# Performance work log

Hardware: AMD Instinct MI355X
Metric: run time of the kernel (lower is better)

The kernel has to match this reference:

```python
import jax, jax.numpy as jnp
import numpy as np

N_ATOMS = 10000
N_PAIR = 100000
F = 128
N_HEAD = 4
FH = F // N_HEAD  # 32
DEGREES = [1, 2, 3]
N_DEG = len(DEGREES)
REPEATS = np.array([2 * l + 1 for l in DEGREES])  # [3,5,7]
M_TOT = int(REPEATS.sum())  # 15
K_RBF = 32


def ssp(x):
    # shifted softplus: softplus(x) - log(2)
    return jax.nn.softplus(x) - jnp.log(2.0).astype(x.dtype)


def setup_inputs() -> dict:
    key = jax.random.key(0)
    ks = jax.random.split(key, 16)
    inp = {
        "x": jax.random.normal(ks[0], (N_ATOMS, F), jnp.float32),
        "rbf_ij": jax.random.normal(ks[1], (N_PAIR, K_RBF), jnp.float32),
        "sph_ij": jax.random.normal(ks[2], (N_PAIR, M_TOT), jnp.float32),
        "phi_r_cut": jax.random.uniform(ks[3], (N_PAIR,), jnp.float32),
        "idx_i": jnp.sort(jax.random.randint(ks[4], (N_PAIR,), 0, N_ATOMS)),
        "idx_j": jax.random.randint(ks[5], (N_PAIR,), 0, N_ATOMS),
        "pair_mask": jnp.ones((N_PAIR,), jnp.float32),
        # params
        "W_Q": jax.random.normal(ks[6], (N_DEG, N_HEAD, FH, FH), jnp.float32) / np.sqrt(FH),
        "W_K": jax.random.normal(ks[7], (N_DEG, N_HEAD, FH, FH), jnp.float32) / np.sqrt(FH),
        # in2f MLP: single dense F -> F
        "W_in": jax.random.normal(ks[8], (F, F), jnp.float32) / np.sqrt(F),
        "b_in": jnp.zeros((F,), jnp.float32),
        # radial filter MLP: K -> K (ssp) -> n_deg*F
        "W_f1": jax.random.normal(ks[9], (K_RBF, K_RBF), jnp.float32) / np.sqrt(K_RBF),
        "b_f1": jnp.zeros((K_RBF,), jnp.float32),
        "W_f2": jax.random.normal(ks[10], (K_RBF, N_DEG * F), jnp.float32) / np.sqrt(K_RBF),
        "b_f2": jnp.zeros((N_DEG * F,), jnp.float32),
        # f2out MLP: single dense F -> F
        "W_out": jax.random.normal(ks[11], (F, F), jnp.float32) / np.sqrt(F),
        "b_out": jnp.zeros((F,), jnp.float32),
    }
    return inp


def reference(x, rbf_ij, sph_ij, phi_r_cut, idx_i, idx_j, pair_mask,
              W_Q, W_K, W_in, b_in, W_f1, b_f1, W_f2, b_f2, W_out, b_out):
    n = x.shape[0]
    # in2f embedding (last in2f dim == F)
    x_f = x @ W_in + b_in                                  # (n, F)
    x_head = x_f.reshape(n, N_HEAD, FH)                    # (n, h, FH)

    # per-degree, per-head linear maps (the nested vmap matmuls)
    Q = jnp.einsum('dhij,nhj->ndhi', W_Q, x_head)          # (n, n_deg, h, FH)
    K = jnp.einsum('dhij,nhj->ndhi', W_K, x_head)

    m = pair_mask[:, None, None, None]
    Q_i = Q[idx_i] * m                                     # (P, n_deg, h, FH)
    K_j = K[idx_j] * m

    # radial filter: MLP(rbf) -> (P, n_deg, h, FH), scaled by cutoff
    h1 = ssp(rbf_ij @ W_f1 + b_f1)
    W_ij = (h1 @ W_f2 + b_f2).reshape(-1, N_DEG, N_HEAD, FH)
    W_ij = W_ij * phi_r_cut[:, None, None, None]

    # attention coefficients per degree/head
    alpha = jnp.sum(Q_i * K_j * W_ij, axis=-1)             # (P, n_deg, h)
    alpha = jnp.repeat(alpha, repeats=REPEATS, axis=1, total_repeat_length=M_TOT)  # (P, m_tot, h)
    alpha = alpha / jnp.sqrt(jnp.asarray(FH, x.dtype))     # att_scale

    # outer product of neighbor features with spherical harmonics
    x_j = x_head[idx_j] * pair_mask[:, None, None]         # (P, h, FH)
    z_ij = jnp.einsum('pm,phf->pmhf', sph_ij, x_j)         # (P, m_tot, h, FH)
    z_ij = alpha[:, :, :, None] * z_ij
    z_ij = z_ij.reshape(z_ij.shape[0], M_TOT, F)           # (P, m_tot, F)

    agg = jax.ops.segment_sum(z_ij, idx_i, num_segments=n)  # (n, m_tot, F)

    # f2out projection (last f2out dim == F)
    out = agg @ W_out + b_out                               # (n, m_tot, F)
    return out
```

## Files before the change

### kernel.cpp

```cpp
#include <hip/hip_runtime.h>
#include <hip/hip_bf16.h>

#define N_ATOMS 10000
#define N_PAIR  100000
#define F_DIM   128
#define N_HEAD  4
#define FH      32
#define N_DEG   3
#define M_TOT   15
#define K_RBF   32
#define R_OUT   (N_ATOMS * M_TOT)
#define PPB     50

typedef __attribute__((ext_vector_type(8))) short short8;
typedef __attribute__((ext_vector_type(4))) float f32x4;

union frag_cast { int i[4]; short8 s; };

__device__ __forceinline__ float sspf(float v) {
    float sp = fmaxf(v, 0.f) + log1pf(expf(-fabsf(v)));
    return sp - 0.69314718055994531f;
}

__device__ __forceinline__ unsigned short bf16_rne(float x) {
    unsigned int u = __float_as_uint(x);
    unsigned int r = u + 0x7fffu + ((u >> 16) & 1u);
    return (unsigned short)(r >> 16);
}
__device__ __forceinline__ float bf16_tof(unsigned short h) {
    return __uint_as_float(((unsigned int)h) << 16);
}

__global__ __launch_bounds__(256) void k_zero(float4* __restrict__ p, int n4)
{
    int i = blockIdx.x * 256 + threadIdx.x;
    int stride = gridDim.x * 256;
    float4 z = make_float4(0.f, 0.f, 0.f, 0.f);
    for (; i < n4; i += stride) p[i] = z;
}

__global__ __launch_bounds__(256) void k_gemm128(
    const float* __restrict__ A, const float* __restrict__ B,
    const float* __restrict__ bias, float* __restrict__ C, int rows)
{
    __shared__ float As[32][132];
    __shared__ float Bs[32][132];
    int r0 = blockIdx.x * 128;
    int t = threadIdx.x;
    int ty = t >> 4, tx = t & 15;

    float acc[8][8];
    #pragma unroll
    for (int i = 0; i < 8; ++i)
        #pragma unroll
        for (int j = 0; j < 8; ++j) acc[i][j] = 0.f;

    for (int k0 = 0; k0 < 128; k0 += 32) {
        #pragma unroll
        for (int r = 0; r < 16; ++r) {
            int idx = t + 256 * r;
            int row = idx >> 5, kk = idx & 31;
            int grow = r0 + row;
            As[kk][row] = (grow < rows) ? A[grow * 128 + k0 + kk] : 0.f;
        }
        #pragma unroll
        for (int r = 0; r < 16; ++r) {
            int idx = t + 256 * r;
            int kk = idx >> 7, c = idx & 127;
            Bs[kk][c] = B[(k0 + kk) * 128 + c];
        }
        __syncthreads();

        #pragma unroll
        for (int kk = 0; kk < 32; ++kk) {
            float a[8], b[8];
            *(float4*)&a[0] = *(const float4*)&As[kk][ty * 4];
            *(float4*)&a[4] = *(const float4*)&As[kk][64 + ty * 4];
            *(float4*)&b[0] = *(const float4*)&Bs[kk][tx * 4];
            *(float4*)&b[4] = *(const float4*)&Bs[kk][64 + tx * 4];
            #pragma unroll
            for (int i = 0; i < 8; ++i)
                #pragma unroll
                for (int j = 0; j < 8; ++j)
                    acc[i][j] = fmaf(a[i], b[j], acc[i][j]);
        }
        __syncthreads();
    }

    float bj[8];
    #pragma unroll
    for (int j = 0; j < 4; ++j) { bj[j] = bias[tx * 4 + j]; bj[4 + j] = bias[64 + tx * 4 + j]; }

    #pragma unroll
    for (int i = 0; i < 8; ++i) {
        int row = r0 + ((i < 4) ? (ty * 4 + i) : (64 + ty * 4 + (i - 4)));
        if (row < rows) {
            float4 v0, v1;
            v0.x = acc[i][0] + bj[0]; v0.y = acc[i][1] + bj[1];
            v0.z = acc[i][2] + bj[2]; v0.w = acc[i][3] + bj[3];
            v1.x = acc[i][4] + bj[4]; v1.y = acc[i][5] + bj[5];
            v1.z = acc[i][6] + bj[6]; v1.w = acc[i][7] + bj[7];
            *(float4*)&C[row * 128 + tx * 4] = v0;
            *(float4*)&C[row * 128 + 64 + tx * 4] = v1;
        }
    }
}

__global__ __launch_bounds__(384) void k_qk(
    const float* __restrict__ xh, const float* __restrict__ W_Q,
    const float* __restrict__ W_K, float* __restrict__ Q, float* __restrict__ K)
{
    __shared__ float xfs[32][128];
    int t = threadIdx.x;
    int h = (t >> 5) & 3;
    float wq[32], wk[32];
    const float4* wqp = (const float4*)(W_Q + t * 32);
    const float4* wkp = (const float4*)(W_K + t * 32);
    #pragma unroll
    for (int j4 = 0; j4 < 8; ++j4) {
        float4 a = wqp[j4], b = wkp[j4];
        wq[4 * j4 + 0] = a.x; wq[4 * j4 + 1] = a.y; wq[4 * j4 + 2] = a.z; wq[4 * j4 + 3] = a.w;
        wk[4 * j4 + 0] = b.x; wk[4 * j4 + 1] = b.y; wk[4 * j4 + 2] = b.z; wk[4 * j4 + 3] = b.w;
    }
    int ab = blockIdx.x * 32;
    for (int idx = t; idx < 4096; idx += 384) {
        int aa = idx >> 7, f = idx & 127;
        int ag = ab + aa;
        xfs[aa][f] = (ag < N_ATOMS) ? xh[ag * 128 + f] : 0.f;
    }
    __syncthreads();
    for (int aa = 0; aa < 32; ++aa) {
        int ag = ab + aa;
        if (ag >= N_ATOMS) break;
        const float4* xv = (const float4*)&xfs[aa][h * 32];
        float q0 = 0.f, q1 = 0.f, k0 = 0.f, k1 = 0.f;
        #pragma unroll
        for (int j4 = 0; j4 < 8; j4 += 2) {
            float4 x0 = xv[j4], x1 = xv[j4 + 1];
            q0 = fmaf(wq[4 * j4 + 0], x0.x, q0); q0 = fmaf(wq[4 * j4 + 1], x0.y, q0);
            q0 = fmaf(wq[4 * j4 + 2], x0.z, q0); q0 = fmaf(wq[4 * j4 + 3], x0.w, q0);
            q1 = fmaf(wq[4 * j4 + 4], x1.x, q1); q1 = fmaf(wq[4 * j4 + 5], x1.y, q1);
            q1 = fmaf(wq[4 * j4 + 6], x1.z, q1); q1 = fmaf(wq[4 * j4 + 7], x1.w, q1);
            k0 = fmaf(wk[4 * j4 + 0], x0.x, k0); k0 = fmaf(wk[4 * j4 + 1], x0.y, k0);
            k0 = fmaf(wk[4 * j4 + 2], x0.z, k0); k0 = fmaf(wk[4 * j4 + 3], x0.w, k0);
            k1 = fmaf(wk[4 * j4 + 4], x1.x, k1); k1 = fmaf(wk[4 * j4 + 5], x1.y, k1);
            k1 = fmaf(wk[4 * j4 + 6], x1.z, k1); k1 = fmaf(wk[4 * j4 + 7], x1.w, k1);
        }
        Q[ag * 384 + t] = q0 + q1;
        K[ag * 384 + t] = k0 + k1;
    }
}

__global__ __launch_bounds__(256) void k_cvt_w2(
    const float* __restrict__ W, unsigned short* __restrict__ Wh,
    unsigned short* __restrict__ Wl)
{
    int idx = blockIdx.x * 256 + threadIdx.x;
    if (idx < 12288) {
        int e = idx >> 5, k = idx & 31;
        float v = W[k * 384 + e];
        unsigned short h = bf16_rne(v);
        unsigned short l = bf16_rne(v - bf16_tof(h));
        Wh[e * 32 + k] = h;
        Wl[e * 32 + k] = l;
    }
}

__global__ __launch_bounds__(256) void k_pair(
    const float* __restrict__ rbf, const float* __restrict__ phi,
    const float* __restrict__ mask, const int* __restrict__ idx_i,
    const int* __restrict__ idx_j, const float* __restrict__ W_f1,
    const float* __restrict__ b_f1, const unsigned short* __restrict__ W2h,
    const unsigned short* __restrict__ W2l, const float* __restrict__ b_f2,
    const float* __restrict__ Q, const float* __restrict__ K,
    float* __restrict__ alpha)
{
    __shared__ float g_s[16][388];
    __shared__ unsigned int h1p_s[16][36];
    __shared__ int   i_s[16];
    __shared__ int   j_s[16];
    __shared__ float phim_s[16];

    float (*rbf_s)[33] = (float (*)[33])(&g_s[0][0]);
    float (*wf1_s)[33] = (float (*)[33])(&g_s[0][0] + 16 * 33);

    int t = threadIdx.x;
    int p0 = blockIdx.x * 16;

    for (int idx = t; idx < 1536; idx += 256) {
        if (idx < 512) {
            rbf_s[idx >> 5][idx & 31] = rbf[p0 * 32 + idx];
        } else {
            int k = idx - 512;
            wf1_s[k >> 5][k & 31] = W_f1[k];
        }
    }
    if (t < 16) {
        int pg = p0 + t;
        i_s[t] = idx_i[pg];
        j_s[t] = idx_j[pg];
        float m = mask[pg];
        phim_s[t] = phi[pg] * m * m * 0.17677669529663687f;
    }
    __syncthreads();

    {
        int p = t >> 4, c0 = (t & 15) * 2;
        float acc0 = b_f1[c0], acc1 = b_f1[c0 + 1];
        #pragma unroll
        for (int k = 0; k < 32; ++k) {
            float rv = rbf_s[p][k];
            acc0 = fmaf(rv, wf1_s[k][c0], acc0);
            acc1 = fmaf(rv, wf1_s[k][c0 + 1], acc1);
        }
        float h0 = sspf(acc0), h1v = sspf(acc1);
        unsigned short hh0 = bf16_rne(h0);
        unsigned short ll0 = bf16_rne(h0 - bf16_tof(hh0));
        unsigned short hh1 = bf16_rne(h1v);
        unsigned short ll1 = bf16_rne(h1v - bf16_tof(hh1));
        h1p_s[p][c0]     = ((unsigned int)hh0 << 16) | (unsigned int)ll0;
        h1p_s[p][c0 + 1] = ((unsigned int)hh1 << 16) | (unsigned int)ll1;
    }
    __syncthreads();

    #pragma unroll
    for (int it = 0; it < 6; ++it) {
        int idx = it * 256 + t;
        int p = idx / 96;
        int c4 = idx - p * 96;
        const float4* qp = (const float4*)(Q + i_s[p] * 384) + c4;
        const float4* kp = (const float4*)(K + j_s[p] * 384) + c4;
        float4 qv = *qp, kv = *kp;
        float4 gv;
        gv.x = qv.x * kv.x; gv.y = qv.y * kv.y;
        gv.z = qv.z * kv.z; gv.w = qv.w * kv.w;
        *(float4*)&g_s[p][c4 * 4] = gv;
    }
    __syncthreads();

    int wave = t >> 6, lane = t & 63;
    int quad = lane >> 4, l15 = lane & 15;

    short8 ah, al;
    {
        const unsigned int* hp = &h1p_s[l15][quad * 8];
        uint4 u01 = *(const uint4*)hp;
        uint4 u23 = *(const uint4*)(hp + 4);
        unsigned int u[8] = {u01.x, u01.y, u01.z, u01.w, u23.x, u23.y, u23.z, u23.w};
        frag_cast fh, fl;
        #pragma unroll
        for (int q = 0; q < 4; ++q) {
            unsigned int a0 = u[2 * q], a1 = u[2 * q + 1];
            fh.i[q] = (int)((a0 >> 16) | (a1 & 0xffff0000u));
            fl.i[q] = (int)((a0 & 0xffffu) | (a1 << 16));
        }
        ah = fh.s;
        al = fl.s;
    }

    #pragma unroll
    for (int dd = 0; dd < 3; ++dd) {
        int dh = wave * 3 + dd;
        int e_base = dh * 32;
        short8 bh0 = *(const short8*)(W2h + (e_base + l15) * 32 + quad * 8);
        short8 bl0 = *(const short8*)(W2l + (e_base + l15) * 32 + quad * 8);
        short8 bh1 = *(const short8*)(W2h + (e_base + 16 + l15) * 32 + quad * 8);
        short8 bl1 = *(const short8*)(W2l + (e_base + 16 + l15) * 32 + quad * 8);
        float b2v0 = b_f2[e_base + l15];
        float b2v1 = b_f2[e_base + 16 + l15];

        f32x4 s0 = {0.f, 0.f, 0.f, 0.f};
        f32x4 s1 = {0.f, 0.f, 0.f, 0.f};
        s0 = __builtin_amdgcn_mfma_f32_16x16x32_bf16(ah, bh0, s0, 0, 0, 0);
        s1 = __builtin_amdgcn_mfma_f32_16x16x32_bf16(ah, bh1, s1, 0, 0, 0);
        s0 = __builtin_amdgcn_mfma_f32_16x16x32_bf16(al, bh0, s0, 0, 0, 0);
        s1 = __builtin_amdgcn_mfma_f32_16x16x32_bf16(al, bh1, s1, 0, 0, 0);
        s0 = __builtin_amdgcn_mfma_f32_16x16x32_bf16(ah, bl0, s0, 0, 0, 0);
        s1 = __builtin_amdgcn_mfma_f32_16x16x32_bf16(ah, bl1, s1, 0, 0, 0);

        float vsum[4];
        #pragma unroll
        for (int r = 0; r < 4; ++r) {
            int prow = quad * 4 + r;
            float v = (s0[r] + b2v0) * g_s[prow][e_base + l15]
                    + (s1[r] + b2v1) * g_s[prow][e_base + 16 + l15];
            #pragma unroll
            for (int off = 8; off >= 1; off >>= 1)
                v += __shfl_xor(v, off, 16);
            vsum[r] = v;
        }
        if (l15 == 0) {
            #pragma unroll
            for (int r = 0; r < 4; ++r) {
                int prow = quad * 4 + r;
                alpha[(p0 + prow) * 12 + dh] = vsum[r] * phim_s[prow];
            }
        }
    }
}

__global__ __launch_bounds__(256) void k_cvt_b(
    const float* __restrict__ W, unsigned short* __restrict__ Bth,
    unsigned short* __restrict__ Btl)
{
    int idx = blockIdx.x * 256 + threadIdx.x;
    int cc = idx >> 7, kk = idx & 127;
    float v = W[kk * 128 + cc];
    unsigned short h = bf16_rne(v);
    unsigned short l = bf16_rne(v - bf16_tof(h));
    Bth[cc * 128 + kk] = h;
    Btl[cc * 128 + kk] = l;
}

__device__ __forceinline__ void flush_acc(float* __restrict__ agg, int a,
                                          const float* acc, int t, bool interior)
{
    float* base = agg + (long)a * (M_TOT * 128) + t;
    if (interior) {
        #pragma unroll
        for (int m = 0; m < M_TOT; ++m) base[m * 128] = acc[m];
    } else {
        #pragma unroll
        for (int m = 0; m < M_TOT; ++m) atomicAdd(&base[m * 128], acc[m]);
    }
}

__global__ __launch_bounds__(512) void k_aggc(
    const float* __restrict__ xh, const float* __restrict__ alpha,
    const float* __restrict__ sph, const int* __restrict__ idx_i,
    const int* __restrict__ idx_j, const float* __restrict__ mask,
    float* __restrict__ agg)
{
    int tid = threadIdx.x;
    int grp = tid >> 7;
    int t   = tid & 127;
    int h   = (t >> 5) & 3;
    int g0  = (blockIdx.x * 4 + grp) * PPB;
    int g1  = g0 + PPB;

    int prevA = (g0 > 0) ? idx_i[g0 - 1] : -1;
    int nextA = (g1 < N_PAIR) ? idx_i[g1] : -1;

    float acc[M_TOT];
    #pragma unroll
    for (int m = 0; m < M_TOT; ++m) acc[m] = 0.f;

    int cur = idx_i[g0];
    bool started_inside = (cur != prevA);

    for (int p = g0; p < g1; ++p) {
        int ii = idx_i[p];
        if (ii != cur) {
            flush_acc(agg, cur, acc, t, started_inside);
            #pragma unroll
            for (int m = 0; m < M_TOT; ++m) acc[m] = 0.f;
            cur = ii;
            started_inside = true;
        }
        int jj = idx_j[p];
        float xj = xh[jj * 128 + t] * mask[p];
        float a0 = alpha[p * 12 + h];
        float a1 = alpha[p * 12 + 4 + h];
        float a2 = alpha[p * 12 + 8 + h];
        const float* sp = sph + p * 15;
        #pragma unroll
        for (int m = 0; m < M_TOT; ++m) {
            float av = (m < 3) ? a0 : ((m < 8) ? a1 : a2);
            acc[m] = fmaf(sp[m] * av, xj, acc[m]);
        }
    }
    bool interior = started_inside && (cur != nextA);
    flush_acc(agg, cur, acc, t, interior);
}

__global__ __launch_bounds__(256) void k_out2(
    const unsigned short* __restrict__ Bth, const unsigned short* __restrict__ Btl,
    const float* __restrict__ bias, float* __restrict__ C)
{
    __shared__ unsigned int ap_s[64][132];
    int tid = threadIdx.x;
    long r0 = (long)blockIdx.x * 64;

    #pragma unroll
    for (int it = 0; it < 16; ++it) {
        int idx = tid + it * 256;
        int row = idx >> 5, c4 = (idx & 31) * 4;
        long gr = r0 + row;
        float4 v = make_float4(0.f, 0.f, 0.f, 0.f);
        if (gr < (long)R_OUT) v = *(const float4*)(C + gr * 128 + c4);
        float vv[4] = {v.x, v.y, v.z, v.w};
        unsigned int pk[4];
        #pragma unroll
        for (int q = 0; q < 4; ++q) {
            unsigned short hh = bf16_rne(vv[q]);
            unsigned short ll = bf16_rne(vv[q] - bf16_tof(hh));
            pk[q] = ((unsigned int)hh << 16) | (unsigned int)ll;
        }
        *(uint4*)&ap_s[row][c4] = make_uint4(pk[0], pk[1], pk[2], pk[3]);
    }
    __syncthreads();

    int wave = tid >> 6, lane = tid & 63;
    int quad = lane >> 4, l15 = lane & 15;

    short8 fa_h[4], fa_l[4];
    #pragma unroll
    for (int ks = 0; ks < 4; ++ks) {
        const unsigned int* hp = &ap_s[wave * 16 + l15][ks * 32 + quad * 8];
        uint4 u01 = *(const uint4*)hp;
        uint4 u23 = *(const uint4*)(hp + 4);
        unsigned int u[8] = {u01.x, u01.y, u01.z, u01.w, u23.x, u23.y, u23.z, u23.w};
        frag_cast fh, fl;
        #pragma unroll
        for (int q = 0; q < 4; ++q) {
            unsigned int a0 = u[2 * q], a1 = u[2 * q + 1];
            fh.i[q] = (int)((a0 >> 16) | (a1 & 0xffff0000u));
            fl.i[q] = (int)((a0 & 0xffffu) | (a1 << 16));
        }
        fa_h[ks] = fh.s;
        fa_l[ks] = fl.s;
    }

    #pragma unroll
    for (int ct = 0; ct < 8; ++ct) {
        int colbase = ct * 16;
        short8 bh[4], bl[4];
        #pragma unroll
        for (int ks = 0; ks < 4; ++ks) {
            int off = (colbase + l15) * 128 + ks * 32 + quad * 8;
            bh[ks] = *(const short8*)(Bth + off);
            bl[ks] = *(const short8*)(Btl + off);
        }
        f32x4 oacc = {0.f, 0.f, 0.f, 0.f};
        #pragma unroll
        for (int ks = 0; ks < 4; ++ks) {
            oacc = __builtin_amdgcn_mfma_f32_16x16x32_bf16(fa_h[ks], bh[ks], oacc, 0, 0, 0);
            oacc = __builtin_amdgcn_mfma_f32_16x16x32_bf16(fa_l[ks], bh[ks], oacc, 0, 0, 0);
            oacc = __builtin_amdgcn_mfma_f32_16x16x32_bf16(fa_h[ks], bl[ks], oacc, 0, 0, 0);
        }
        float bv = bias[colbase + l15];
        #pragma unroll
        for (int r = 0; r < 4; ++r) {
            long row = r0 + wave * 16 + quad * 4 + r;
            if (row < (long)R_OUT)
                C[row * 128 + colbase + l15] = oacc[r] + bv;
        }
    }
}

extern "C" void kernel_launch(void* const* d_in, const int* in_sizes, int n_in,
                              void* d_out, int out_size, void* d_ws, size_t ws_size,
                              hipStream_t stream) {
    const float* x        = (const float*)d_in[0];
    const float* rbf_ij   = (const float*)d_in[1];
    const float* sph_ij   = (const float*)d_in[2];
    const float* phi_r    = (const float*)d_in[3];
    const int*   idx_i    = (const int*)d_in[4];
    const int*   idx_j    = (const int*)d_in[5];
    const float* pmask    = (const float*)d_in[6];
    const float* W_Q      = (const float*)d_in[7];
    const float* W_K      = (const float*)d_in[8];
    const float* W_in     = (const float*)d_in[9];
    const float* b_in     = (const float*)d_in[10];
    const float* W_f1     = (const float*)d_in[11];
    const float* b_f1     = (const float*)d_in[12];
    const float* W_f2     = (const float*)d_in[13];
    const float* b_f2     = (const float*)d_in[14];
    const float* W_out    = (const float*)d_in[15];
    const float* b_out    = (const float*)d_in[16];
    float* out = (float*)d_out;

    float* ws    = (float*)d_ws;
    float* xh    = ws;
    float* Qbuf  = xh + N_ATOMS * F_DIM;
    float* Kbuf  = Qbuf + N_ATOMS * 384;
    float* alpha = Kbuf + N_ATOMS * 384;
    unsigned short* Bth = (unsigned short*)(alpha + N_PAIR * 12);
    unsigned short* Btl = Bth + 16384;
    unsigned short* W2h = Btl + 16384;
    unsigned short* W2l = W2h + 12288;

    k_zero<<<2048, 256, 0, stream>>>((float4*)d_out, R_OUT * 128 / 4);
    k_cvt_b<<<64, 256, 0, stream>>>(W_out, Bth, Btl);
    k_cvt_w2<<<48, 256, 0, stream>>>(W_f2, W2h, W2l);
    k_gemm128<<<(N_ATOMS + 127) / 128, 256, 0, stream>>>(x, W_in, b_in, xh, N_ATOMS);
    k_qk<<<(N_ATOMS + 31) / 32, 384, 0, stream>>>(xh, W_Q, W_K, Qbuf, Kbuf);
    k_pair<<<N_PAIR / 16, 256, 0, stream>>>(rbf_ij, phi_r, pmask, idx_i, idx_j,
                                            W_f1, b_f1, W2h, W2l, b_f2,
                                            Qbuf, Kbuf, alpha);
    k_aggc<<<N_PAIR / (4 * PPB), 512, 0, stream>>>(xh, alpha, sph_ij, idx_i, idx_j,
                                                   pmask, out);
    k_out2<<<(R_OUT + 63) / 64, 256, 0, stream>>>(Bth, Btl, b_out, out);
}
```

Measured before the change: 440.0 us.

## Fold output projection into per-atom features before aggregation

Uses linearity to apply W_out per head to each atom's features (x_head · W_out rows) once per atom, producing a 4x128 table per atom. The aggregation kernel then combines the per-head projected features with alpha and writes the final output directly with the bias pre-initialized, removing the 150k×128×128 output GEMM pass and its read/write of the full output. The cost is a larger gather per pair (4x128 floats instead of 128) and extra per-pair FMAs; the output buffer is pre-filled with the bias, so boundary atomics add onto it.

```diff
diff --git a/kernel.cpp b/kernel.cpp
--- a/kernel.cpp
+++ b/kernel.cpp
@@ -31,12 +31,15 @@
     return __uint_as_float(((unsigned int)h) << 16);
 }
 
-__global__ __launch_bounds__(256) void k_zero(float4* __restrict__ p, int n4)
+__global__ __launch_bounds__(256) void k_binit(
+    const float* __restrict__ b, float4* __restrict__ out, int n4)
 {
     int i = blockIdx.x * 256 + threadIdx.x;
     int stride = gridDim.x * 256;
-    float4 z = make_float4(0.f, 0.f, 0.f, 0.f);
-    for (; i < n4; i += stride) p[i] = z;
+    for (; i < n4; i += stride) {
+        int c4 = i & 31;
+        out[i] = *(const float4*)(b + c4 * 4);
+    }
 }
 
 __global__ __launch_bounds__(256) void k_gemm128(
@@ -299,26 +302,57 @@
     }
 }
 
-__global__ __launch_bounds__(256) void k_cvt_b(
-    const float* __restrict__ W, unsigned short* __restrict__ Bth,
-    unsigned short* __restrict__ Btl)
-{
-    int idx = blockIdx.x * 256 + threadIdx.x;
-    int cc = idx >> 7, kk = idx & 127;
-    float v = W[kk * 128 + cc];
-    unsigned short h = bf16_rne(v);
-    unsigned short l = bf16_rne(v - bf16_tof(h));
-    Bth[cc * 128 + kk] = h;
-    Btl[cc * 128 + kk] = l;
-}
-
-__device__ __forceinline__ void flush_acc(float* __restrict__ agg, int a,
-                                          const float* acc, int t, bool interior)
-{
-    float* base = agg + (long)a * (M_TOT * 128) + t;
+__global__ __launch_bounds__(256) void k_xw(
+    const float* __restrict__ xh, const float* __restrict__ W,
+    float* __restrict__ xwh)
+{
+    __shared__ float xs[32][132];
+    int t = threadIdx.x;
+    int a0 = blockIdx.x * 32;
+    #pragma unroll
+    for (int it = 0; it < 4; ++it) {
+        int idx = t + it * 256;
+        int row = idx >> 5, c4 = (idx & 31) * 4;
+        int ga = a0 + row;
+        float4 v = make_float4(0.f, 0.f, 0.f, 0.f);
+        if (ga < N_ATOMS) v = *(const float4*)(xh + ga * 128 + c4);
+        *(float4*)&xs[row][c4] = v;
+    }
+    __syncthreads();
+
+    int c = t & 127;
+    int half = t >> 7;
+    #pragma unroll
+    for (int h = 0; h < 4; ++h) {
+        float w[32];
+        #pragma unroll
+        for (int k = 0; k < 32; ++k) w[k] = W[(h * 32 + k) * 128 + c];
+        float acc[16];
+        #pragma unroll
+        for (int i = 0; i < 16; ++i) acc[i] = 0.f;
+        #pragma unroll
+        for (int k = 0; k < 32; ++k) {
+            float wv = w[k];
+            #pragma unroll
+            for (int i = 0; i < 16; ++i)
+                acc[i] = fmaf(xs[half * 16 + i][h * 32 + k], wv, acc[i]);
+        }
+        #pragma unroll
+        for (int i = 0; i < 16; ++i) {
+            int ga = a0 + half * 16 + i;
+            if (ga < N_ATOMS) xwh[(long)ga * 512 + h * 128 + c] = acc[i];
+        }
+    }
+}
+
+__device__ __forceinline__ void flush_acc(float* __restrict__ out, int a,
+                                          const float* acc, float bout,
+                                          int t, bool interior)
+{
+    float* base = out + (long)a * (M_TOT * 128) + t;
     if (interior) {
         #pragma unroll
-        for (int m = 0; m < M_TOT; ++m) base[m * 128] = acc[m];
+        for (int m = 0; m < M_TOT; ++m) base[m * 128] = acc[m] + bout;
     } else {
         #pragma unroll
         for (int m = 0; m < M_TOT; ++m) atomicAdd(&base[m * 128], acc[m]);
@@ -326,18 +360,18 @@
 }
 
 __global__ __launch_bounds__(512) void k_aggc(
-    const float* __restrict__ xh, const float* __restrict__ alpha,
+    const float* __restrict__ xwh, const float* __restrict__ alpha,
     const float* __restrict__ sph, const int* __restrict__ idx_i,
     const int* __restrict__ idx_j, const float* __restrict__ mask,
-    float* __restrict__ agg)
+    const float* __restrict__ b_out, float* __restrict__ out)
 {
     int tid = threadIdx.x;
     int grp = tid >> 7;
     int t   = tid & 127;
-    int h   = (t >> 5) & 3;
     int g0  = (blockIdx.x * 4 + grp) * PPB;
     int g1  = g0 + PPB;
 
+    float bout = b_out[t];
     int prevA = (g0 > 0) ? idx_i[g0 - 1] : -1;
     int nextA = (g1 < N_PAIR) ? idx_i[g1] : -1;
 
@@ -351,101 +385,32 @@
     for (int p = g0; p < g1; ++p) {
         int ii = idx_i[p];
         if (ii != cur) {
-            flush_acc(agg, cur, acc, t, started_inside);
+            flush_acc(out, cur, acc, bout, t, started_inside);
             #pragma unroll
             for (int m = 0; m < M_TOT; ++m) acc[m] = 0.f;
             cur = ii;
             started_inside = true;
         }
         int jj = idx_j[p];
-        float xj = xh[jj * 128 + t] * mask[p];
-        float a0 = alpha[p * 12 + h];
-        float a1 = alpha[p * 12 + 4 + h];
-        float a2 = alpha[p * 12 + 8 + h];
+        const float* xp = xwh + (long)jj * 512;
+        float xw0 = xp[t];
+        float xw1 = xp[128 + t];
+        float xw2 = xp[256 + t];
+        float xw3 = xp[384 + t];
+        float mv = mask[p];
+        const float* ap = alpha + p * 12;
+        float sd0 = (ap[0] * xw0 + ap[1] * xw1 + ap[2]  * xw2 + ap[3]  * xw3) * mv;
+        float sd1 = (ap[4] * xw0 + ap[5] * xw1 + ap[6]  * xw2 + ap[7]  * xw3) * mv;
+        float sd2 = (ap[8] * xw0 + ap[9] * xw1 + ap[10] * xw2 + ap[11] * xw3) * mv;
         const float* sp = sph + p * 15;
         #pragma unroll
         for (int m = 0; m < M_TOT; ++m) {
-            float av = (m < 3) ? a0 : ((m < 8) ? a1 : a2);
-            acc[m] = fmaf(sp[m] * av, xj, acc[m]);
+            float sdv = (m < 3) ? sd0 : ((m < 8) ? sd1 : sd2);
+            acc[m] = fmaf(sp[m], sdv, acc[m]);
         }
     }
     bool interior = started_inside && (cur != nextA);
-    flush_acc(agg, cur, acc, t, interior);
-}
-
-__global__ __launch_bounds__(256) void k_out2(
-    const unsigned short* __restrict__ Bth, const unsigned short* __restrict__ Btl,
-    const float* __restrict__ bias, float* __restrict__ C)
-{
-    __shared__ unsigned int ap_s[64][132];
-    int tid = threadIdx.x;
-    long r0 = (long)blockIdx.x * 64;
-
-    #pragma unroll
-    for (int it = 0; it < 16; ++it) {
-        int idx = tid + it * 256;
-        int row = idx >> 5, c4 = (idx & 31) * 4;
-        long gr = r0 + row;
-        float4 v = make_float4(0.f, 0.f, 0.f, 0.f);
-        if (gr < (long)R_OUT) v = *(const float4*)(C + gr * 128 + c4);
-        float vv[4] = {v.x, v.y, v.z, v.w};
-        unsigned int pk[4];
-        #pragma unroll
-        for (int q = 0; q < 4; ++q) {
-            unsigned short hh = bf16_rne(vv[q]);
-            unsigned short ll = bf16_rne(vv[q] - bf16_tof(hh));
-            pk[q] = ((unsigned int)hh << 16) | (unsigned int)ll;
-        }
-        *(uint4*)&ap_s[row][c4] = make_uint4(pk[0], pk[1], pk[2], pk[3]);
-    }
-    __syncthreads();
-
-    int wave = tid >> 6, lane = tid & 63;
-    int quad = lane >> 4, l15 = lane & 15;
-
-    short8 fa_h[4], fa_l[4];
-    #pragma unroll
-    for (int ks = 0; ks < 4; ++ks) {
-        const unsigned int* hp = &ap_s[wave * 16 + l15][ks * 32 + quad * 8];
-        uint4 u01 = *(const uint4*)hp;
-        uint4 u23 = *(const uint4*)(hp + 4);
-        unsigned int u[8] = {u01.x, u01.y, u01.z, u01.w, u23.x, u23.y, u23.z, u23.w};
-        frag_cast fh, fl;
-        #pragma unroll
-        for (int q = 0; q < 4; ++q) {
-            unsigned int a0 = u[2 * q], a1 = u[2 * q + 1];
-            fh.i[q] = (int)((a0 >> 16) | (a1 & 0xffff0000u));
-            fl.i[q] = (int)((a0 & 0xffffu) | (a1 << 16));
-        }
-        fa_h[ks] = fh.s;
-        fa_l[ks] = fl.s;
-    }
-
-    #pragma unroll
-    for (int ct = 0; ct < 8; ++ct) {
-        int colbase = ct * 16;
-        short8 bh[4], bl[4];
-        #pragma unroll
-        for (int ks = 0; ks < 4; ++ks) {
-            int off = (colbase + l15) * 128 + ks * 32 + quad * 8;
-            bh[ks] = *(const short8*)(Bth + off);
-            bl[ks] = *(const short8*)(Btl + off);
-        }
-        f32x4 oacc = {0.f, 0.f, 0.f, 0.f};
-        #pragma unroll
-        for (int ks = 0; ks < 4; ++ks) {
-            oacc = __builtin_amdgcn_mfma_f32_16x16x32_bf16(fa_h[ks], bh[ks], oacc, 0, 0, 0);
-            oacc = __builtin_amdgcn_mfma_f32_16x16x32_bf16(fa_l[ks], bh[ks], oacc, 0, 0, 0);
-            oacc = __builtin_amdgcn_mfma_f32_16x16x32_bf16(fa_h[ks], bl[ks], oacc, 0, 0, 0);
-        }
-        float bv = bias[colbase + l15];
-        #pragma unroll
-        for (int r = 0; r < 4; ++r) {
-            long row = r0 + wave * 16 + quad * 4 + r;
-            if (row < (long)R_OUT)
-                C[row * 128 + colbase + l15] = oacc[r] + bv;
-        }
-    }
+    flush_acc(out, cur, acc, bout, t, interior);
 }
 
 extern "C" void kernel_launch(void* const* d_in, const int* in_sizes, int n_in,
@@ -475,20 +440,18 @@
     float* Qbuf  = xh + N_ATOMS * F_DIM;
     float* Kbuf  = Qbuf + N_ATOMS * 384;
     float* alpha = Kbuf + N_ATOMS * 384;
-    unsigned short* Bth = (unsigned short*)(alpha + N_PAIR * 12);
-    unsigned short* Btl = Bth + 16384;
-    unsigned short* W2h = Btl + 16384;
+    unsigned short* W2h = (unsigned short*)(alpha + N_PAIR * 12);
     unsigned short* W2l = W2h + 12288;
-
-    k_zero<<<2048, 256, 0, stream>>>((float4*)d_out, R_OUT * 128 / 4);
-    k_cvt_b<<<64, 256, 0, stream>>>(W_out, Bth, Btl);
+    float* xwh   = Qbuf;
+
+    k_binit<<<2048, 256, 0, stream>>>(b_out, (float4*)d_out, R_OUT * 128 / 4);
     k_cvt_w2<<<48, 256, 0, stream>>>(W_f2, W2h, W2l);
     k_gemm128<<<(N_ATOMS + 127) / 128, 256, 0, stream>>>(x, W_in, b_in, xh, N_ATOMS);
     k_qk<<<(N_ATOMS + 31) / 32, 384, 0, stream>>>(xh, W_Q, W_K, Qbuf, Kbuf);
     k_pair<<<N_PAIR / 16, 256, 0, stream>>>(rbf_ij, phi_r, pmask, idx_i, idx_j,
                                             W_f1, b_f1, W2h, W2l, b_f2,
                                             Qbuf, Kbuf, alpha);
-    k_aggc<<<N_PAIR / (4 * PPB), 512, 0, stream>>>(xh, alpha, sph_ij, idx_i, idx_j,
-                                                   pmask, out);
-    k_out2<<<(R_OUT + 63) / 64, 256, 0, stream>>>(Bth, Btl, b_out, out);
-}
+    k_xw<<<(N_ATOMS + 31) / 32, 256, 0, stream>>>(xh, W_out, xwh);
+    k_aggc<<<N_PAIR / (4 * PPB), 512, 0, stream>>>(xwh, alpha, sph_ij, idx_i, idx_j,
+                                                   pmask, b_out, out);
+}
```

Result: faster. 414.7 us (-5.7%).
